# Kernel optimization log

Hardware: AMD Instinct MI355X
Metric: run time of the kernel (lower is better)

Reference implementation:

```python
import jax, jax.numpy as jnp
import numpy as np

E = 8        # n_experts
H = 1024     # hidden_size == input_size
M = 2048     # intermediate_size
K = 2        # topk
SE = 1       # share_expert
BSZ, SEQ = 2, 1024
W_SCALE = 0.02


def setup_inputs() -> dict:
    key = jax.random.key(0)
    ks = jax.random.split(key, 9)
    return {
        "x": jax.random.normal(ks[0], (BSZ, SEQ, H), jnp.float32),
        "gate_w": jax.random.normal(ks[1], (E, H), jnp.float32) * W_SCALE,
        "beta": jnp.zeros((E,), jnp.float32),
        "gate_proj_w": jax.random.normal(ks[2], (E, H, M), jnp.float32) * W_SCALE,
        "up_proj_w": jax.random.normal(ks[3], (E, H, M), jnp.float32) * W_SCALE,
        "down_proj_w": jax.random.normal(ks[4], (E, M, H), jnp.float32) * W_SCALE,
        "shared_gate_w": jax.random.normal(ks[5], (SE, H, M), jnp.float32) * W_SCALE,
        "shared_up_w": jax.random.normal(ks[6], (SE, H, M), jnp.float32) * W_SCALE,
        "shared_down_w": jax.random.normal(ks[7], (SE, M, H), jnp.float32) * W_SCALE,
    }


def reference(x, gate_w, beta, gate_proj_w, up_proj_w, down_proj_w,
              shared_gate_w, shared_up_w, shared_down_w):
    B0, S0, H0 = x.shape
    xt = x.reshape(-1, H0)                       # [B, H], B = B0*S0 tokens
    B = xt.shape[0]

    # --- routing: top-k on (logits + beta), gate prob = sigmoid(selected logits) ---
    logits = xt @ gate_w.T                       # [B, E]
    _, idx = jax.lax.top_k(logits + beta, K)     # [B, K] expert indices
    probs = jax.nn.sigmoid(jnp.take_along_axis(logits, idx, axis=-1))  # [B, K]

    # combine weights c[b, e]: scatter top-k probs (equivalent to index_add combine)
    c = jnp.zeros((B, E), xt.dtype).at[jnp.arange(B)[:, None], idx].add(probs)

    # --- per-expert SwiGLU over all tokens, then weighted combine by c ---
    g = jnp.einsum('bh,ehm->bem', xt, gate_proj_w)   # [B, E, M]
    u = jnp.einsum('bh,ehm->bem', xt, up_proj_w)     # [B, E, M]
    h = jax.nn.silu(g) * u                           # [B, E, M]
    eo = jnp.einsum('bem,emh->beh', h, down_proj_w)  # [B, E, H]
    combined = jnp.einsum('beh,be->bh', eo, c)       # [B, H]

    # --- shared expert(s): applied to every token, no gating ---
    sg = jnp.einsum('bh,ehm->bem', xt, shared_gate_w)
    su = jnp.einsum('bh,ehm->bem', xt, shared_up_w)
    sh = jax.nn.silu(sg) * su
    shared_out = jnp.einsum('bem,emh->beh', sh, shared_down_w).sum(axis=1)  # [B, H]

    return (combined + shared_out).reshape(B0, S0, H0)
```

## Files before the change

### kernel.cpp

```cpp
#include <hip/hip_runtime.h>

#define NE 8
#define HD 1024
#define MD 2048
#define NT 2048
#define NSH 4096

typedef __attribute__((ext_vector_type(8))) short s16x8;
typedef __attribute__((ext_vector_type(4))) float f32x4;
typedef __attribute__((ext_vector_type(8))) unsigned short u16x8;
typedef __attribute__((ext_vector_type(4))) unsigned short u16x4;

__device__ __forceinline__ unsigned short f2bf(float f) {
    union { float f; unsigned int i; } v; v.f = f;
    unsigned int u = v.i;
    return (unsigned short)((u + 0x7FFFu + ((u >> 16) & 1u)) >> 16);
}
__device__ __forceinline__ float bf2f(unsigned short u) {
    union { unsigned int i; float f; } v; v.i = ((unsigned int)u) << 16; return v.f;
}

__device__ __forceinline__ void gld16(const unsigned short* g, short* l) {
    __builtin_amdgcn_global_load_lds(
        (const __attribute__((address_space(1))) unsigned int*)g,
        (__attribute__((address_space(3))) unsigned int*)l,
        16, 0, 0);
}

__global__ __launch_bounds__(256) void k_cvt(
    const float* __restrict__ s, unsigned short* __restrict__ d, int n)
{
    int i = (blockIdx.x * 256 + threadIdx.x) * 4;
    int stride = gridDim.x * 256 * 4;
    for (; i < n; i += stride) {
        float4 v = *(const float4*)(s + i);
        u16x4 o;
        o[0] = f2bf(v.x); o[1] = f2bf(v.y); o[2] = f2bf(v.z); o[3] = f2bf(v.w);
        *(u16x4*)(d + i) = o;
    }
}

__global__ __launch_bounds__(256) void k_cvt_t(
    const float* __restrict__ wr, const float* __restrict__ wsd,
    unsigned short* __restrict__ o, int K, int N)
{
    int e = blockIdx.z;
    const float* src = (e < NE) ? wr + (size_t)e * K * N : wsd;
    unsigned short* dst = o + (size_t)e * N * K;
    int k0 = blockIdx.x * 32, n0 = blockIdx.y * 128;
    __shared__ float T[32 * 132];
    int tid = threadIdx.x;
    #pragma unroll
    for (int p = 0; p < 4; p++) {
        int k = (tid >> 5) + p * 8;
        int n4 = (tid & 31) * 4;
        float4 v = *(const float4*)(src + (size_t)(k0 + k) * N + n0 + n4);
        *(float4*)(&T[k * 132 + n4]) = v;
    }
    __syncthreads();
    #pragma unroll
    for (int p = 0; p < 2; p++) {
        int idx = tid + p * 256;
        int n = idx >> 2;
        int kq = (idx & 3) * 8;
        u16x8 r;
        #pragma unroll
        for (int j = 0; j < 8; j++) r[j] = f2bf(T[(kq + j) * 132 + n]);
        *(u16x8*)(dst + (size_t)(n0 + n) * K + k0 + kq) = r;
    }
}

__global__ __launch_bounds__(256) void k_route(
    const float* __restrict__ x, const float* __restrict__ gw,
    const float* __restrict__ beta,
    int* __restrict__ cnt, int* __restrict__ list, int* __restrict__ slot,
    float* __restrict__ rprob)
{
    int wave = threadIdx.x >> 6, lane = threadIdx.x & 63;
    int t = blockIdx.x * 4 + wave;
    const float4* xp = (const float4*)(x + (size_t)t * HD) + lane * 4;
    float4 xv[4];
    #pragma unroll
    for (int j = 0; j < 4; j++) xv[j] = xp[j];

    float logit[NE];
    #pragma unroll
    for (int e = 0; e < NE; e++) {
        const float4* gp = (const float4*)(gw + e * HD) + lane * 4;
        float s = 0.f;
        #pragma unroll
        for (int j = 0; j < 4; j++) {
            float4 g = gp[j];
            s += xv[j].x * g.x + xv[j].y * g.y + xv[j].z * g.z + xv[j].w * g.w;
        }
        for (int off = 32; off > 0; off >>= 1) s += __shfl_xor(s, off);
        logit[e] = s;
    }
    if (lane == 0) {
        float v[NE];
        #pragma unroll
        for (int e = 0; e < NE; e++) v[e] = logit[e] + beta[e];
        int i1 = 0; float m1 = v[0];
        #pragma unroll
        for (int e = 1; e < NE; e++) if (v[e] > m1) { m1 = v[e]; i1 = e; }
        int i2 = -1; float m2 = -3.4e38f;
        #pragma unroll
        for (int e = 0; e < NE; e++) if (e != i1 && v[e] > m2) { m2 = v[e]; i2 = e; }
        if (i2 < 0) i2 = (i1 + 1) & 7;
        float p1 = 1.f / (1.f + __expf(-logit[i1]));
        float p2 = 1.f / (1.f + __expf(-logit[i2]));
        int pos1 = atomicAdd(cnt + i1, 1);
        list[i1 * NT + pos1] = t; slot[t * 2 + 0] = (i1 << 16) | pos1; rprob[t * 2 + 0] = p1;
        int pos2 = atomicAdd(cnt + i2, 1);
        list[i2 * NT + pos2] = t; slot[t * 2 + 1] = (i2 << 16) | pos2; rprob[t * 2 + 1] = p2;
    }
}

__global__ void k_scan(const int* __restrict__ cnt, int* __restrict__ base) {
    if (threadIdx.x == 0) {
        int run = 0;
        for (int e = 0; e < NE; e++) { base[e] = run; run += cnt[e]; }
        base[NE] = run;
    }
}

__global__ __launch_bounds__(256) void k_gateup(
    const unsigned short* __restrict__ x,
    const unsigned short* __restrict__ wg_all, const unsigned short* __restrict__ wu_all,
    const int* __restrict__ cnt, const int* __restrict__ base, const int* __restrict__ list,
    unsigned short* __restrict__ h)
{
    int e = blockIdx.z;
    int i0 = blockIdx.y * 128;
    int n0 = blockIdx.x * 128;
    int cnte = (e < NE) ? cnt[e] : NT;
    if (i0 >= cnte) return;
    int rbase = (e < NE) ? base[e] : NSH;
    const unsigned short* wg = wg_all + (size_t)e * HD * MD;
    const unsigned short* wu = wu_all + (size_t)e * HD * MD;

    __shared__ short As[2][128 * 32];
    __shared__ short Bg[2][128 * 32];
    __shared__ short Bu[2][128 * 32];
    __shared__ int tok[128];

    int tid = threadIdx.x;
    int lane = tid & 63, wave = tid >> 6;
    if (tid < 128) {
        int gi = i0 + tid;
        tok[tid] = (e < NE) ? ((gi < cnte) ? list[e * NT + gi] : list[e * NT]) : gi;
    }
    __syncthreads();

    int rr = wave * 32 + (lane >> 2);
    int kc = (lane & 3) * 8;
    size_t gaA0 = (size_t)tok[rr] * HD + kc;
    size_t gaA1 = (size_t)tok[rr + 16] * HD + kc;
    size_t gaB0 = (size_t)(n0 + rr) * HD + kc;
    size_t gaB1 = (size_t)(n0 + rr + 16) * HD + kc;
    int lo0 = (wave * 32) * 32, lo1 = (wave * 32 + 16) * 32;

    int wr = (wave >> 1) * 64, wc = (wave & 1) * 64;
    int m = lane & 15, q = lane >> 4;

    f32x4 accG[4][4], accU[4][4];
    #pragma unroll
    for (int a = 0; a < 4; a++)
        #pragma unroll
        for (int b = 0; b < 4; b++) { accG[a][b] = (f32x4)0.f; accU[a][b] = (f32x4)0.f; }

    gld16(x + gaA0, &As[0][lo0]);
    gld16(x + gaA1, &As[0][lo1]);
    gld16(wg + gaB0, &Bg[0][lo0]);
    gld16(wg + gaB1, &Bg[0][lo1]);
    gld16(wu + gaB0, &Bu[0][lo0]);
    gld16(wu + gaB1, &Bu[0][lo1]);

    int it = 0;
    for (int k0 = 0; k0 < HD; k0 += 32, it ^= 1) {
        __syncthreads();
        int nk = k0 + 32;
        if (nk < HD) {
            int nb = it ^ 1;
            gld16(x + gaA0 + nk, &As[nb][lo0]);
            gld16(x + gaA1 + nk, &As[nb][lo1]);
            gld16(wg + gaB0 + nk, &Bg[nb][lo0]);
            gld16(wg + gaB1 + nk, &Bg[nb][lo1]);
            gld16(wu + gaB0 + nk, &Bu[nb][lo0]);
            gld16(wu + gaB1 + nk, &Bu[nb][lo1]);
        }
        s16x8 af[4];
        #pragma unroll
        for (int ti = 0; ti < 4; ti++)
            af[ti] = *(const s16x8*)(&As[it][(wr + ti * 16 + m) * 32 + q * 8]);
        #pragma unroll
        for (int tj = 0; tj < 4; tj++) {
            int nn = wc + tj * 16 + m;
            s16x8 bg = *(const s16x8*)(&Bg[it][nn * 32 + q * 8]);
            s16x8 bu = *(const s16x8*)(&Bu[it][nn * 32 + q * 8]);
            #pragma unroll
            for (int ti = 0; ti < 4; ti++) {
                accG[ti][tj] = __builtin_amdgcn_mfma_f32_16x16x32_bf16(af[ti], bg, accG[ti][tj], 0, 0, 0);
                accU[ti][tj] = __builtin_amdgcn_mfma_f32_16x16x32_bf16(af[ti], bu, accU[ti][tj], 0, 0, 0);
            }
        }
    }
    #pragma unroll
    for (int ti = 0; ti < 4; ti++)
        #pragma unroll
        for (int tj = 0; tj < 4; tj++)
            #pragma unroll
            for (int r = 0; r < 4; r++) {
                int gi = i0 + wr + ti * 16 + q * 4 + r;
                if (gi < cnte) {
                    int col = n0 + wc + tj * 16 + m;
                    float g = accG[ti][tj][r], u = accU[ti][tj][r];
                    float hv = (g / (1.f + __expf(-g))) * u;
                    h[(size_t)(rbase + gi) * MD + col] = f2bf(hv);
                }
            }
}

__global__ __launch_bounds__(256) void k_down(
    const unsigned short* __restrict__ wd_all,
    const int* __restrict__ cnt, const int* __restrict__ base,
    const unsigned short* __restrict__ h, unsigned short* __restrict__ eo)
{
    int e = blockIdx.z;
    int i0 = blockIdx.y * 128;
    int n0 = blockIdx.x * 128;
    int cnte = (e < NE) ? cnt[e] : NT;
    if (i0 >= cnte) return;
    int rbase = (e < NE) ? base[e] : NSH;
    const unsigned short* wd = wd_all + (size_t)e * MD * HD;

    __shared__ short As[2][128 * 32];
    __shared__ short Bd[2][128 * 32];

    int tid = threadIdx.x;
    int lane = tid & 63, wave = tid >> 6;
    int rr = wave * 32 + (lane >> 2);
    int kc = (lane & 3) * 8;
    size_t gaA0 = (size_t)(rbase + i0 + rr) * MD + kc;
    size_t gaA1 = (size_t)(rbase + i0 + rr + 16) * MD + kc;
    size_t gaB0 = (size_t)(n0 + rr) * MD + kc;
    size_t gaB1 = (size_t)(n0 + rr + 16) * MD + kc;
    int lo0 = (wave * 32) * 32, lo1 = (wave * 32 + 16) * 32;

    int wr = (wave >> 1) * 64, wc = (wave & 1) * 64;
    int m = lane & 15, q = lane >> 4;

    f32x4 acc[4][4];
    #pragma unroll
    for (int a = 0; a < 4; a++)
        #pragma unroll
        for (int b = 0; b < 4; b++) acc[a][b] = (f32x4)0.f;

    gld16(h + gaA0, &As[0][lo0]);
    gld16(h + gaA1, &As[0][lo1]);
    gld16(wd + gaB0, &Bd[0][lo0]);
    gld16(wd + gaB1, &Bd[0][lo1]);

    int it = 0;
    for (int k0 = 0; k0 < MD; k0 += 32, it ^= 1) {
        __syncthreads();
        int nk = k0 + 32;
        if (nk < MD) {
            int nb = it ^ 1;
            gld16(h + gaA0 + nk, &As[nb][lo0]);
            gld16(h + gaA1 + nk, &As[nb][lo1]);
            gld16(wd + gaB0 + nk, &Bd[nb][lo0]);
            gld16(wd + gaB1 + nk, &Bd[nb][lo1]);
        }
        s16x8 af[4];
        #pragma unroll
        for (int ti = 0; ti < 4; ti++)
            af[ti] = *(const s16x8*)(&As[it][(wr + ti * 16 + m) * 32 + q * 8]);
        #pragma unroll
        for (int tj = 0; tj < 4; tj++) {
            int nn = wc + tj * 16 + m;
            s16x8 bd = *(const s16x8*)(&Bd[it][nn * 32 + q * 8]);
            #pragma unroll
            for (int ti = 0; ti < 4; ti++)
                acc[ti][tj] = __builtin_amdgcn_mfma_f32_16x16x32_bf16(af[ti], bd, acc[ti][tj], 0, 0, 0);
        }
    }
    #pragma unroll
    for (int ti = 0; ti < 4; ti++)
        #pragma unroll
        for (int tj = 0; tj < 4; tj++)
            #pragma unroll
            for (int r = 0; r < 4; r++) {
                int gi = i0 + wr + ti * 16 + q * 4 + r;
                if (gi < cnte) {
                    int col = n0 + wc + tj * 16 + m;
                    eo[(size_t)(rbase + gi) * HD + col] = f2bf(acc[ti][tj][r]);
                }
            }
}

__global__ __launch_bounds__(256) void k_combine(
    const unsigned short* __restrict__ eo, const int* __restrict__ slot,
    const float* __restrict__ rprob, const int* __restrict__ base,
    float* __restrict__ out)
{
    int t = blockIdx.x;
    int s0 = slot[t * 2], s1 = slot[t * 2 + 1];
    float p0 = rprob[t * 2], p1 = rprob[t * 2 + 1];
    int r0 = base[s0 >> 16] + (s0 & 0xFFFF);
    int r1 = base[s1 >> 16] + (s1 & 0xFFFF);
    int rs = NSH + t;
    int c = threadIdx.x * 4;
    u16x4 a = *(const u16x4*)(eo + (size_t)r0 * HD + c);
    u16x4 b = *(const u16x4*)(eo + (size_t)r1 * HD + c);
    u16x4 s = *(const u16x4*)(eo + (size_t)rs * HD + c);
    float4 res;
    res.x = p0 * bf2f(a[0]) + p1 * bf2f(b[0]) + bf2f(s[0]);
    res.y = p0 * bf2f(a[1]) + p1 * bf2f(b[1]) + bf2f(s[1]);
    res.z = p0 * bf2f(a[2]) + p1 * bf2f(b[2]) + bf2f(s[2]);
    res.w = p0 * bf2f(a[3]) + p1 * bf2f(b[3]) + bf2f(s[3]);
    *(float4*)(out + (size_t)t * HD + c) = res;
}

extern "C" void kernel_launch(void* const* d_in, const int* in_sizes, int n_in,
                              void* d_out, int out_size, void* d_ws, size_t ws_size,
                              hipStream_t stream)
{
    const float* x    = (const float*)d_in[0];
    const float* gw   = (const float*)d_in[1];
    const float* beta = (const float*)d_in[2];
    const float* wg   = (const float*)d_in[3];
    const float* wu   = (const float*)d_in[4];
    const float* wd   = (const float*)d_in[5];
    const float* swg  = (const float*)d_in[6];
    const float* swu  = (const float*)d_in[7];
    const float* swd  = (const float*)d_in[8];
    float* out = (float*)d_out;

    char* ws = (char*)d_ws;
    const size_t MB = (size_t)1 << 20;
    int*   cnt   = (int*)(ws + 0);
    int*   basep = (int*)(ws + 64);
    int*   list  = (int*)(ws + 1024);
    int*   slot  = (int*)(ws + 1024 + 65536);
    float* rprob = (float*)(ws + 1024 + 65536 + 16384);
    unsigned short* xb  = (unsigned short*)(ws + 1 * MB);
    unsigned short* wgt = (unsigned short*)(ws + 8 * MB);
    unsigned short* wut = (unsigned short*)(ws + 46 * MB);
    unsigned short* wdt = (unsigned short*)(ws + 84 * MB);
    unsigned short* h   = (unsigned short*)(ws + 122 * MB);
    unsigned short* eo  = (unsigned short*)(ws + 146 * MB);

    hipMemsetAsync(ws, 0, 128, stream);

    const int NX = NT * HD;
    k_cvt<<<512, 256, 0, stream>>>(x, xb, NX);

    dim3 tgu(HD / 32, MD / 128, NE + 1);
    k_cvt_t<<<tgu, 256, 0, stream>>>(wg, swg, wgt, HD, MD);
    k_cvt_t<<<tgu, 256, 0, stream>>>(wu, swu, wut, HD, MD);
    dim3 td(MD / 32, HD / 128, NE + 1);
    k_cvt_t<<<td, 256, 0, stream>>>(wd, swd, wdt, MD, HD);

    k_route<<<NT / 4, 256, 0, stream>>>(x, gw, beta, cnt, list, slot, rprob);
    k_scan<<<1, 64, 0, stream>>>(cnt, basep);

    dim3 g3(MD / 128, NT / 128, NE + 1);
    k_gateup<<<g3, 256, 0, stream>>>(xb, wgt, wut, cnt, basep, list, h);

    dim3 g4(HD / 128, NT / 128, NE + 1);
    k_down<<<g4, 256, 0, stream>>>(wdt, cnt, basep, h, eo);

    k_combine<<<NT, 256, 0, stream>>>(eo, slot, rprob, basep, out);
}
```

Before: 508.4 us.

## Interleave gate/up weights into one GEMM, swizzle LDS, raise occupancy

The gate and up weights are written into a single row-interleaved bf16 buffer, so gate_up runs as one GEMM with N = 2*MD, half the accumulators and one B tile per block. The silu*up product is formed through a lane shuffle in the epilogue, with only even lanes writing h. LDS reads and global_load_lds destinations get an XOR swizzle on the k-chunk to cut bank conflicts, and both GEMM kernels gain a launch-bounds occupancy hint of 4. The grid doubles in blocks, and each block now writes only half-width columns, which could hurt store coalescing.

```diff
diff --git a/kernel.cpp b/kernel.cpp
--- a/kernel.cpp
+++ b/kernel.cpp
@@ -42,11 +42,11 @@
 
 __global__ __launch_bounds__(256) void k_cvt_t(
     const float* __restrict__ wr, const float* __restrict__ wsd,
-    unsigned short* __restrict__ o, int K, int N)
+    unsigned short* __restrict__ o, int K, int N, int rstride, int roff)
 {
     int e = blockIdx.z;
     const float* src = (e < NE) ? wr + (size_t)e * K * N : wsd;
-    unsigned short* dst = o + (size_t)e * N * K;
+    unsigned short* dst = o + (size_t)e * N * K * rstride;
     int k0 = blockIdx.x * 32, n0 = blockIdx.y * 128;
     __shared__ float T[32 * 132];
     int tid = threadIdx.x;
@@ -66,7 +66,7 @@
         u16x8 r;
         #pragma unroll
         for (int j = 0; j < 8; j++) r[j] = f2bf(T[(kq + j) * 132 + n]);
-        *(u16x8*)(dst + (size_t)(n0 + n) * K + k0 + kq) = r;
+        *(u16x8*)(dst + ((size_t)(n0 + n) * rstride + roff) * K + k0 + kq) = r;
     }
 }
 
@@ -124,9 +124,9 @@
     }
 }
 
-__global__ __launch_bounds__(256) void k_gateup(
+__global__ __launch_bounds__(256, 4) void k_gateup(
     const unsigned short* __restrict__ x,
-    const unsigned short* __restrict__ wg_all, const unsigned short* __restrict__ wu_all,
+    const unsigned short* __restrict__ wgu,
     const int* __restrict__ cnt, const int* __restrict__ base, const int* __restrict__ list,
     unsigned short* __restrict__ h)
 {
@@ -136,12 +136,10 @@
     int cnte = (e < NE) ? cnt[e] : NT;
     if (i0 >= cnte) return;
     int rbase = (e < NE) ? base[e] : NSH;
-    const unsigned short* wg = wg_all + (size_t)e * HD * MD;
-    const unsigned short* wu = wu_all + (size_t)e * HD * MD;
+    const unsigned short* wb = wgu + (size_t)e * (2 * MD) * HD;
 
     __shared__ short As[2][128 * 32];
-    __shared__ short Bg[2][128 * 32];
-    __shared__ short Bu[2][128 * 32];
+    __shared__ short Bs[2][128 * 32];
     __shared__ int tok[128];
 
     int tid = threadIdx.x;
@@ -153,7 +151,7 @@
     __syncthreads();
 
     int rr = wave * 32 + (lane >> 2);
-    int kc = (lane & 3) * 8;
+    int kc = ((lane & 3) ^ ((lane >> 3) & 3)) * 8;
     size_t gaA0 = (size_t)tok[rr] * HD + kc;
     size_t gaA1 = (size_t)tok[rr + 16] * HD + kc;
     size_t gaB0 = (size_t)(n0 + rr) * HD + kc;
@@ -162,19 +160,18 @@
 
     int wr = (wave >> 1) * 64, wc = (wave & 1) * 64;
     int m = lane & 15, q = lane >> 4;
-
-    f32x4 accG[4][4], accU[4][4];
+    int sa = (m >> 1) & 3;
+
+    f32x4 acc[4][4];
     #pragma unroll
     for (int a = 0; a < 4; a++)
         #pragma unroll
-        for (int b = 0; b < 4; b++) { accG[a][b] = (f32x4)0.f; accU[a][b] = (f32x4)0.f; }
+        for (int b = 0; b < 4; b++) acc[a][b] = (f32x4)0.f;
 
     gld16(x + gaA0, &As[0][lo0]);
     gld16(x + gaA1, &As[0][lo1]);
-    gld16(wg + gaB0, &Bg[0][lo0]);
-    gld16(wg + gaB1, &Bg[0][lo1]);
-    gld16(wu + gaB0, &Bu[0][lo0]);
-    gld16(wu + gaB1, &Bu[0][lo1]);
+    gld16(wb + gaB0, &Bs[0][lo0]);
+    gld16(wb + gaB1, &Bs[0][lo1]);
 
     int it = 0;
     for (int k0 = 0; k0 < HD; k0 += 32, it ^= 1) {
@@ -184,25 +181,20 @@
             int nb = it ^ 1;
             gld16(x + gaA0 + nk, &As[nb][lo0]);
             gld16(x + gaA1 + nk, &As[nb][lo1]);
-            gld16(wg + gaB0 + nk, &Bg[nb][lo0]);
-            gld16(wg + gaB1 + nk, &Bg[nb][lo1]);
-            gld16(wu + gaB0 + nk, &Bu[nb][lo0]);
-            gld16(wu + gaB1 + nk, &Bu[nb][lo1]);
+            gld16(wb + gaB0 + nk, &Bs[nb][lo0]);
+            gld16(wb + gaB1 + nk, &Bs[nb][lo1]);
         }
         s16x8 af[4];
         #pragma unroll
         for (int ti = 0; ti < 4; ti++)
-            af[ti] = *(const s16x8*)(&As[it][(wr + ti * 16 + m) * 32 + q * 8]);
+            af[ti] = *(const s16x8*)(&As[it][(wr + ti * 16 + m) * 32 + (q ^ sa) * 8]);
         #pragma unroll
         for (int tj = 0; tj < 4; tj++) {
             int nn = wc + tj * 16 + m;
-            s16x8 bg = *(const s16x8*)(&Bg[it][nn * 32 + q * 8]);
-            s16x8 bu = *(const s16x8*)(&Bu[it][nn * 32 + q * 8]);
+            s16x8 bf = *(const s16x8*)(&Bs[it][nn * 32 + (q ^ sa) * 8]);
             #pragma unroll
-            for (int ti = 0; ti < 4; ti++) {
-                accG[ti][tj] = __builtin_amdgcn_mfma_f32_16x16x32_bf16(af[ti], bg, accG[ti][tj], 0, 0, 0);
-                accU[ti][tj] = __builtin_amdgcn_mfma_f32_16x16x32_bf16(af[ti], bu, accU[ti][tj], 0, 0, 0);
-            }
+            for (int ti = 0; ti < 4; ti++)
+                acc[ti][tj] = __builtin_amdgcn_mfma_f32_16x16x32_bf16(af[ti], bf, acc[ti][tj], 0, 0, 0);
         }
     }
     #pragma unroll
@@ -211,17 +203,19 @@
         for (int tj = 0; tj < 4; tj++)
             #pragma unroll
             for (int r = 0; r < 4; r++) {
+                float v = acc[ti][tj][r];
+                float uo = __shfl_xor(v, 1);
                 int gi = i0 + wr + ti * 16 + q * 4 + r;
-                if (gi < cnte) {
-                    int col = n0 + wc + tj * 16 + m;
-                    float g = accG[ti][tj][r], u = accU[ti][tj][r];
-                    float hv = (g / (1.f + __expf(-g))) * u;
-                    h[(size_t)(rbase + gi) * MD + col] = f2bf(hv);
+                if (!(m & 1) && gi < cnte) {
+                    float g = v;
+                    float hv = (g / (1.f + __expf(-g))) * uo;
+                    int colI = n0 + wc + tj * 16 + m;
+                    h[(size_t)(rbase + gi) * MD + (colI >> 1)] = f2bf(hv);
                 }
             }
 }
 
-__global__ __launch_bounds__(256) void k_down(
+__global__ __launch_bounds__(256, 4) void k_down(
     const unsigned short* __restrict__ wd_all,
     const int* __restrict__ cnt, const int* __restrict__ base,
     const unsigned short* __restrict__ h, unsigned short* __restrict__ eo)
@@ -240,7 +234,7 @@
     int tid = threadIdx.x;
     int lane = tid & 63, wave = tid >> 6;
     int rr = wave * 32 + (lane >> 2);
-    int kc = (lane & 3) * 8;
+    int kc = ((lane & 3) ^ ((lane >> 3) & 3)) * 8;
     size_t gaA0 = (size_t)(rbase + i0 + rr) * MD + kc;
     size_t gaA1 = (size_t)(rbase + i0 + rr + 16) * MD + kc;
     size_t gaB0 = (size_t)(n0 + rr) * MD + kc;
@@ -249,6 +243,7 @@
 
     int wr = (wave >> 1) * 64, wc = (wave & 1) * 64;
     int m = lane & 15, q = lane >> 4;
+    int sa = (m >> 1) & 3;
 
     f32x4 acc[4][4];
     #pragma unroll
@@ -275,11 +270,11 @@
         s16x8 af[4];
         #pragma unroll
         for (int ti = 0; ti < 4; ti++)
-            af[ti] = *(const s16x8*)(&As[it][(wr + ti * 16 + m) * 32 + q * 8]);
+            af[ti] = *(const s16x8*)(&As[it][(wr + ti * 16 + m) * 32 + (q ^ sa) * 8]);
         #pragma unroll
         for (int tj = 0; tj < 4; tj++) {
             int nn = wc + tj * 16 + m;
-            s16x8 bd = *(const s16x8*)(&Bd[it][nn * 32 + q * 8]);
+            s16x8 bd = *(const s16x8*)(&Bd[it][nn * 32 + (q ^ sa) * 8]);
             #pragma unroll
             for (int ti = 0; ti < 4; ti++)
                 acc[ti][tj] = __builtin_amdgcn_mfma_f32_16x16x32_bf16(af[ti], bd, acc[ti][tj], 0, 0, 0);
@@ -344,12 +339,11 @@
     int*   list  = (int*)(ws + 1024);
     int*   slot  = (int*)(ws + 1024 + 65536);
     float* rprob = (float*)(ws + 1024 + 65536 + 16384);
-    unsigned short* xb  = (unsigned short*)(ws + 1 * MB);
-    unsigned short* wgt = (unsigned short*)(ws + 8 * MB);
-    unsigned short* wut = (unsigned short*)(ws + 46 * MB);
-    unsigned short* wdt = (unsigned short*)(ws + 84 * MB);
-    unsigned short* h   = (unsigned short*)(ws + 122 * MB);
-    unsigned short* eo  = (unsigned short*)(ws + 146 * MB);
+    unsigned short* xb   = (unsigned short*)(ws + 1 * MB);
+    unsigned short* wgut = (unsigned short*)(ws + 8 * MB);
+    unsigned short* wdt  = (unsigned short*)(ws + 84 * MB);
+    unsigned short* h    = (unsigned short*)(ws + 122 * MB);
+    unsigned short* eo   = (unsigned short*)(ws + 146 * MB);
 
     hipMemsetAsync(ws, 0, 128, stream);
 
@@ -357,16 +351,16 @@
     k_cvt<<<512, 256, 0, stream>>>(x, xb, NX);
 
     dim3 tgu(HD / 32, MD / 128, NE + 1);
-    k_cvt_t<<<tgu, 256, 0, stream>>>(wg, swg, wgt, HD, MD);
-    k_cvt_t<<<tgu, 256, 0, stream>>>(wu, swu, wut, HD, MD);
+    k_cvt_t<<<tgu, 256, 0, stream>>>(wg, swg, wgut, HD, MD, 2, 0);
+    k_cvt_t<<<tgu, 256, 0, stream>>>(wu, swu, wgut, HD, MD, 2, 1);
     dim3 td(MD / 32, HD / 128, NE + 1);
-    k_cvt_t<<<td, 256, 0, stream>>>(wd, swd, wdt, MD, HD);
+    k_cvt_t<<<td, 256, 0, stream>>>(wd, swd, wdt, MD, HD, 1, 0);
 
     k_route<<<NT / 4, 256, 0, stream>>>(x, gw, beta, cnt, list, slot, rprob);
     k_scan<<<1, 64, 0, stream>>>(cnt, basep);
 
-    dim3 g3(MD / 128, NT / 128, NE + 1);
-    k_gateup<<<g3, 256, 0, stream>>>(xb, wgt, wut, cnt, basep, list, h);
+    dim3 g3(2 * MD / 128, NT / 128, NE + 1);
+    k_gateup<<<g3, 256, 0, stream>>>(xb, wgut, cnt, basep, list, h);
 
     dim3 g4(HD / 128, NT / 128, NE + 1);
     k_down<<<g4, 256, 0, stream>>>(wdt, cnt, basep, h, eo);
```

Result: faster. 476.0 us (-6.4%).
